# Optimization experiments

Hardware: AMD Instinct MI355X
Metric: run time of the kernel (lower is better)

## Reference

```python
import jax, jax.numpy as jnp
import numpy as np

N = 100000   # num_nodes
E = 1600000  # num_edges (avg degree 16)
IN = 128     # input_dim
H = 4        # num_heads
D = 32       # hidden_dim per head (H*D == 128)
NEG_SLOPE = 0.2


def setup_inputs() -> dict:
    key = jax.random.key(0)
    ks = jax.random.split(key, 8)
    s = 0.1
    x = jax.random.normal(ks[0], (N, IN), jnp.float32)
    edge_index = jax.random.randint(ks[1], (2, E), 0, N, dtype=jnp.int32)
    W_gat = jax.random.normal(ks[2], (H * D, IN), jnp.float32) * s   # GATConv lin weight
    att_src = jax.random.normal(ks[3], (H, D), jnp.float32) * s
    att_dst = jax.random.normal(ks[4], (H, D), jnp.float32) * s
    bias_gat = jnp.zeros((H * D,), jnp.float32)
    W_lin = jax.random.normal(ks[5], (IN, H * D), jnp.float32) * s   # nn.Linear weight
    b_lin = jnp.zeros((IN,), jnp.float32)
    return {"x": x, "edge_index": edge_index, "W_gat": W_gat,
            "att_src": att_src, "att_dst": att_dst, "bias_gat": bias_gat,
            "W_lin": W_lin, "b_lin": b_lin}


def reference(x, edge_index, W_gat, att_src, att_dst, bias_gat, W_lin, b_lin):
    # (eval mode: all dropouts are identity; sparse edge weights unused in original)
    h = (x @ W_gat.T).reshape(N, H, D)                 # [N,H,D] per-head projections
    a_s = jnp.einsum('nhd,hd->nh', h, att_src)         # [N,H]
    a_d = jnp.einsum('nhd,hd->nh', h, att_dst)         # [N,H]
    # add self loops (PyG default)
    loop = jnp.arange(N, dtype=edge_index.dtype)
    src = jnp.concatenate([edge_index[0], loop])       # [E+N]
    dst = jnp.concatenate([edge_index[1], loop])       # [E+N]
    logits = jax.nn.leaky_relu(a_s[src] + a_d[dst], NEG_SLOPE)  # [E+N,H]
    # segment softmax over edges grouped by destination node
    m = jax.ops.segment_max(logits, dst, num_segments=N)        # [N,H]
    e = jnp.exp(logits - m[dst])
    denom = jax.ops.segment_sum(e, dst, num_segments=N)         # [N,H]
    alpha = e / denom[dst]                                      # [E+N,H]
    # scatter-aggregate weighted source features
    agg = jax.ops.segment_sum(alpha[:, :, None] * h[src], dst, num_segments=N)
    out = agg.reshape(N, H * D) + bias_gat             # concat heads + bias
    out = jax.nn.relu(out)
    return out @ W_lin.T + b_lin                       # [N, IN]
```

## Files before the change

### kernel.cpp

```cpp
#include <hip/hip_runtime.h>
#include <hip/hip_bf16.h>
#include <hip/hip_fp16.h>

#define NN 100000
#define EE 1600000
#define INF_DIM 128
#define NHEAD 4
#define HDIM 32
#define NEG_SLOPE 0.2f

#define GB 1024

typedef __attribute__((ext_vector_type(8))) short short8;
typedef __attribute__((ext_vector_type(4))) float floatx4;

__device__ __forceinline__ unsigned int cvtpk_bf16(float lo, float hi) {
  unsigned int r;
  asm("v_cvt_pk_bf16_f32 %0, %1, %2" : "=v"(r) : "v"(lo), "v"(hi));
  return r;
}
__device__ __forceinline__ unsigned int packh2(float a, float b) {
  const __half ha = __float2half(a), hb = __float2half(b);
  const unsigned short ua = *(const unsigned short*)&ha;
  const unsigned short ub = *(const unsigned short*)&hb;
  return (unsigned int)ua | ((unsigned int)ub << 16);
}
__device__ __forceinline__ float pickw(const int4 e, const int head) {
  const unsigned int d = (head & 2) ? (unsigned int)e.z : (unsigned int)e.y;
  const unsigned short us =
      (head & 1) ? (unsigned short)(d >> 16) : (unsigned short)(d & 0xffffu);
  const __half h = *(const __half*)&us;
  return __half2float(h);
}
__device__ __forceinline__ void accum8h(const uint4 g, const float c,
                                        float* acc) {
  union { uint4 u; __half2 h[4]; } v;
  v.u = g;
#pragma unroll
  for (int j = 0; j < 4; ++j) {
    const float2 f = __half22float2(v.h[j]);
    acc[2 * j] = fmaf(c, f.x, acc[2 * j]);
    acc[2 * j + 1] = fmaf(c, f.y, acc[2 * j + 1]);
  }
}

#define LDA 136

__global__ __launch_bounds__(256) void gemm_mfma(
    const float* __restrict__ Af, const unsigned short* __restrict__ Ab,
    const float* __restrict__ W, const float* __restrict__ bias,
    unsigned short* __restrict__ Ch, float* __restrict__ Cf,
    const float* __restrict__ att_src, const float* __restrict__ att_dst,
    float* __restrict__ a_s, float* __restrict__ a_d,
    const int* __restrict__ dstE, int* __restrict__ deg8, int M) {
  __shared__ unsigned short sW[128 * LDA];
  const int tid = threadIdx.x;

  if (dstE) {
    int* mydeg = deg8 + (size_t)(blockIdx.x & 7) * NN;
    for (int e = blockIdx.x * 256 + tid; e < EE; e += GB * 256)
      atomicAdd(&mydeg[dstE[e]], 1);
  }

  {
    const int r = tid >> 1;
    const int c0 = (tid & 1) * 64;
#pragma unroll
    for (int j = 0; j < 16; ++j) {
      const float4 v = *(const float4*)&W[r * 128 + c0 + j * 4];
      uint2 u;
      u.x = cvtpk_bf16(v.x, v.y);
      u.y = cvtpk_bf16(v.z, v.w);
      *(uint2*)&sW[r * LDA + c0 + j * 4] = u;
    }
  }
  __syncthreads();

  const int wv = tid >> 6;
  const int lane = tid & 63;
  const int l16 = lane & 15;
  const int quad = lane >> 4;
  const int ntiles = (M + 63) >> 6;

  float avs[8], avd[8];
  if (a_s) {
#pragma unroll
    for (int nt = 0; nt < 8; ++nt) {
      avs[nt] = att_src[nt * 16 + l16];
      avd[nt] = att_dst[nt * 16 + l16];
    }
  }

  const unsigned short* wBase = &sW[l16 * LDA + quad * 8];

  for (int t = blockIdx.x; t < ntiles; t += GB) {
    const int m0 = t * 64;
    const int arow = m0 + wv * 16 + l16;
    const int arowc = arow < M ? arow : M - 1;

    short8 af[4];
    if (Af) {
      const float* ap = &Af[(size_t)arowc * 128 + quad * 8];
#pragma unroll
      for (int kc = 0; kc < 4; ++kc) {
        const float4 v0 = *(const float4*)(ap + kc * 32);
        const float4 v1 = *(const float4*)(ap + kc * 32 + 4);
        union { uint4 u; short8 s; } c;
        c.u.x = cvtpk_bf16(v0.x, v0.y);
        c.u.y = cvtpk_bf16(v0.z, v0.w);
        c.u.z = cvtpk_bf16(v1.x, v1.y);
        c.u.w = cvtpk_bf16(v1.z, v1.w);
        af[kc] = c.s;
      }
    } else {
      const unsigned short* ap = &Ab[(size_t)arowc * 128 + quad * 8];
#pragma unroll
      for (int kc = 0; kc < 4; ++kc) af[kc] = *(const short8*)(ap + kc * 32);
    }

    floatx4 acc[8];
#pragma unroll
    for (int i = 0; i < 8; ++i) acc[i] = (floatx4){0.f, 0.f, 0.f, 0.f};

#pragma unroll
    for (int kc = 0; kc < 4; ++kc) {
#pragma unroll
      for (int nt = 0; nt < 8; ++nt) {
        const short8 bfrag = *(const short8*)(wBase + nt * 16 * LDA + kc * 32);
        acc[nt] = __builtin_amdgcn_mfma_f32_16x16x32_bf16(af[kc], bfrag,
                                                          acc[nt], 0, 0, 0);
      }
    }

    const int mrow = m0 + wv * 16 + quad * 4;
#pragma unroll
    for (int nt = 0; nt < 8; ++nt) {
      const int col = nt * 16 + l16;
      const float bv = Cf ? bias[col] : 0.f;
#pragma unroll
      for (int r = 0; r < 4; ++r) {
        const int gm = mrow + r;
        if (gm < M) {
          const float v = acc[nt][r];
          if (Ch) {
            const __half hh = __float2half(v);
            Ch[(size_t)gm * 128 + col] = *(const unsigned short*)&hh;
          } else {
            Cf[(size_t)gm * 128 + col] = v + bv;
          }
        }
      }
    }

    if (a_s) {
#pragma unroll
      for (int r = 0; r < 4; ++r) {
        float ps0 = acc[0][r] * avs[0] + acc[1][r] * avs[1];
        float ps1 = acc[2][r] * avs[2] + acc[3][r] * avs[3];
        float ps2 = acc[4][r] * avs[4] + acc[5][r] * avs[5];
        float ps3 = acc[6][r] * avs[6] + acc[7][r] * avs[7];
        float pd0 = acc[0][r] * avd[0] + acc[1][r] * avd[1];
        float pd1 = acc[2][r] * avd[2] + acc[3][r] * avd[3];
        float pd2 = acc[4][r] * avd[4] + acc[5][r] * avd[5];
        float pd3 = acc[6][r] * avd[6] + acc[7][r] * avd[7];
#pragma unroll
        for (int off = 1; off < 16; off <<= 1) {
          ps0 += __shfl_xor(ps0, off);
          ps1 += __shfl_xor(ps1, off);
          ps2 += __shfl_xor(ps2, off);
          ps3 += __shfl_xor(ps3, off);
          pd0 += __shfl_xor(pd0, off);
          pd1 += __shfl_xor(pd1, off);
          pd2 += __shfl_xor(pd2, off);
          pd3 += __shfl_xor(pd3, off);
        }
        const int gm = mrow + r;
        if (gm < M) {
          const int hs = l16 & 3;
          float vs = ps0;
          if (hs == 1) vs = ps1;
          if (hs == 2) vs = ps2;
          if (hs == 3) vs = ps3;
          float vd = pd0;
          if (hs == 1) vd = pd1;
          if (hs == 2) vd = pd2;
          if (hs == 3) vd = pd3;
          if (l16 < 4)
            a_s[gm * 4 + hs] = vs;
          else if (l16 < 8)
            a_d[gm * 4 + hs] = vd;
        }
      }
    }
  }
}

__global__ __launch_bounds__(256) void alloc_kernel(
    const int* __restrict__ deg8, int* __restrict__ deg,
    int* __restrict__ rowptr, int* __restrict__ cur,
    int* __restrict__ counter) {
  const int i = blockIdx.x * blockDim.x + threadIdx.x;
  const int lane = threadIdx.x & 63;
  int d = 0;
  if (i < NN) {
#pragma unroll
    for (int k = 0; k < 8; ++k) d += deg8[(size_t)k * NN + i];
  }
  int s = d;
#pragma unroll
  for (int off = 1; off < 64; off <<= 1) {
    const int v = __shfl_up(s, off, 64);
    if (lane >= off) s += v;
  }
  const int total = __shfl(s, 63, 64);
  int base = 0;
  if (lane == 63) base = atomicAdd(counter, total);
  base = __shfl(base, 63, 64);
  const int p = base + s - d;
  if (i < NN) {
    rowptr[i] = p;
    cur[i] = p;
    deg[i] = d;
  }
}

__global__ void scatter_kernel(const int* __restrict__ src,
                               const int* __restrict__ dst,
                               const float* __restrict__ a_s,
                               const float* __restrict__ a_d,
                               int* __restrict__ cur, int4* __restrict__ ebuf) {
  const int iA = blockIdx.x * blockDim.x + threadIdx.x;
  const int iB = iA + (EE / 2);
  const int sA_ = src[iA];
  const int dA = dst[iA];
  const int sB_ = src[iB];
  const int dB = dst[iB];
  const int pA = atomicAdd(&cur[dA], 1);
  const int pB = atomicAdd(&cur[dB], 1);
  const float4 asA = *(const float4*)&a_s[sA_ * 4];
  const float4 adA = *(const float4*)&a_d[dA * 4];
  const float4 asB = *(const float4*)&a_s[sB_ * 4];
  const float4 adB = *(const float4*)&a_d[dB * 4];
  float4 lA, lB;
  lA.x = asA.x + adA.x;
  lA.y = asA.y + adA.y;
  lA.z = asA.z + adA.z;
  lA.w = asA.w + adA.w;
  lB.x = asB.x + adB.x;
  lB.y = asB.y + adB.y;
  lB.z = asB.z + adB.z;
  lB.w = asB.w + adB.w;
  lA.x = lA.x > 0.f ? lA.x : NEG_SLOPE * lA.x;
  lA.y = lA.y > 0.f ? lA.y : NEG_SLOPE * lA.y;
  lA.z = lA.z > 0.f ? lA.z : NEG_SLOPE * lA.z;
  lA.w = lA.w > 0.f ? lA.w : NEG_SLOPE * lA.w;
  lB.x = lB.x > 0.f ? lB.x : NEG_SLOPE * lB.x;
  lB.y = lB.y > 0.f ? lB.y : NEG_SLOPE * lB.y;
  lB.z = lB.z > 0.f ? lB.z : NEG_SLOPE * lB.z;
  lB.w = lB.w > 0.f ? lB.w : NEG_SLOPE * lB.w;
  int4 eA, eB;
  eA.x = sA_;
  eA.y = (int)packh2(__expf(lA.x), __expf(lA.y));
  eA.z = (int)packh2(__expf(lA.z), __expf(lA.w));
  eA.w = 0;
  eB.x = sB_;
  eB.y = (int)packh2(__expf(lB.x), __expf(lB.y));
  eB.z = (int)packh2(__expf(lB.z), __expf(lB.w));
  eB.w = 0;
  ebuf[pA] = eA;
  ebuf[pB] = eB;
}

__global__ __launch_bounds__(256) void aggregate_kernel(
    const uint4* __restrict__ hbd4, const float* __restrict__ a_s,
    const float* __restrict__ a_d, const float* __restrict__ bias_gat,
    const int* __restrict__ rowptr, const int* __restrict__ deg,
    const int4* __restrict__ ebuf, uint4* __restrict__ obd4) {
  const int wave = (blockIdx.x * blockDim.x + threadIdx.x) >> 6;
  if (wave >= NN) return;
  const int lane = threadIdx.x & 63;
  const int q = lane >> 4;
  const int f = lane & 15;
  const int head = f >> 2;
  const int n = wave;

  float acc[8];
  float ds;
  {
    const float l0 = a_s[n * 4 + head] + a_d[n * 4 + head];
    const float l = fmaxf(l0, NEG_SLOPE * l0);
    float cs = __expf(l);
    if (q != 0) cs = 0.f;
    union { uint4 u; __half2 h[4]; } v;
    v.u = hbd4[(size_t)n * 16 + f];
#pragma unroll
    for (int j = 0; j < 4; ++j) {
      const float2 fv = __half22float2(v.h[j]);
      acc[2 * j] = cs * fv.x;
      acc[2 * j + 1] = cs * fv.y;
    }
    ds = cs;
  }

  const int beg = rowptr[n];
  const int end = beg + deg[n];
  for (int i = beg; i < end; i += 16) {
    int4 e0, e1, e2, e3;
    {
      const int i0 = i + q, i1 = i + 4 + q, i2 = i + 8 + q, i3 = i + 12 + q;
      e0 = ebuf[i0 < end ? i0 : end - 1];
      e1 = ebuf[i1 < end ? i1 : end - 1];
      e2 = ebuf[i2 < end ? i2 : end - 1];
      e3 = ebuf[i3 < end ? i3 : end - 1];
    }
    const uint4 g0 = hbd4[(size_t)e0.x * 16 + f];
    const uint4 g1 = hbd4[(size_t)e1.x * 16 + f];
    const uint4 g2 = hbd4[(size_t)e2.x * 16 + f];
    const uint4 g3 = hbd4[(size_t)e3.x * 16 + f];
    float c0 = pickw(e0, head);
    float c1 = pickw(e1, head);
    float c2 = pickw(e2, head);
    float c3 = pickw(e3, head);
    if (i + q >= end) c0 = 0.f;
    if (i + 4 + q >= end) c1 = 0.f;
    if (i + 8 + q >= end) c2 = 0.f;
    if (i + 12 + q >= end) c3 = 0.f;
    accum8h(g0, c0, acc);
    accum8h(g1, c1, acc);
    accum8h(g2, c2, acc);
    accum8h(g3, c3, acc);
    ds += c0 + c1 + c2 + c3;
  }

#pragma unroll
  for (int j = 0; j < 8; ++j) {
    acc[j] += __shfl_xor(acc[j], 16);
    acc[j] += __shfl_xor(acc[j], 32);
  }
  ds += __shfl_xor(ds, 16);
  ds += __shfl_xor(ds, 32);

  if (q == 0) {
    const float inv = 1.0f / ds;
    const float4 b0 = *(const float4*)&bias_gat[f * 8];
    const float4 b1 = *(const float4*)&bias_gat[f * 8 + 4];
    float v0 = acc[0] * inv + b0.x;
    float v1 = acc[1] * inv + b0.y;
    float v2 = acc[2] * inv + b0.z;
    float v3 = acc[3] * inv + b0.w;
    float v4 = acc[4] * inv + b1.x;
    float v5 = acc[5] * inv + b1.y;
    float v6 = acc[6] * inv + b1.z;
    float v7 = acc[7] * inv + b1.w;
    v0 = v0 > 0.f ? v0 : 0.f;
    v1 = v1 > 0.f ? v1 : 0.f;
    v2 = v2 > 0.f ? v2 : 0.f;
    v3 = v3 > 0.f ? v3 : 0.f;
    v4 = v4 > 0.f ? v4 : 0.f;
    v5 = v5 > 0.f ? v5 : 0.f;
    v6 = v6 > 0.f ? v6 : 0.f;
    v7 = v7 > 0.f ? v7 : 0.f;
    uint4 r;
    r.x = cvtpk_bf16(v0, v1);
    r.y = cvtpk_bf16(v2, v3);
    r.z = cvtpk_bf16(v4, v5);
    r.w = cvtpk_bf16(v6, v7);
    obd4[(size_t)n * 16 + f] = r;
  }
}

extern "C" void kernel_launch(void* const* d_in, const int* in_sizes, int n_in,
                              void* d_out, int out_size, void* d_ws,
                              size_t ws_size, hipStream_t stream) {
  const float* x = (const float*)d_in[0];
  const int* ei = (const int*)d_in[1];
  const float* W_gat = (const float*)d_in[2];
  const float* att_src = (const float*)d_in[3];
  const float* att_dst = (const float*)d_in[4];
  const float* bias_gat = (const float*)d_in[5];
  const float* W_lin = (const float*)d_in[6];
  const float* b_lin = (const float*)d_in[7];
  float* out = (float*)d_out;

  char* ws = (char*)d_ws;
  size_t off = 0;
  unsigned short* hb = (unsigned short*)(ws + off);
  off += (size_t)NN * 128 * 2;
  unsigned short* ob = (unsigned short*)(ws + off);
  off += (size_t)NN * 128 * 2;
  float* a_s = (float*)(ws + off); off += (size_t)NN * 4 * 4;
  float* a_d = (float*)(ws + off); off += (size_t)NN * 4 * 4;
  int* deg8 = (int*)(ws + off); off += (size_t)8 * NN * 4;
  int* deg = (int*)(ws + off); off += (size_t)NN * 4;
  int* rowptr = (int*)(ws + off); off += (size_t)(NN + 4) * 4;
  int* cur = (int*)(ws + off); off += (size_t)NN * 4;
  int* counter = (int*)(ws + off); off += 16;
  int4* ebuf = (int4*)(ws + off); off += (size_t)EE * 16;

  const int* src = ei;
  const int* dst = ei + EE;

  hipMemsetAsync(deg8, 0, (size_t)8 * NN * 4, stream);
  hipMemsetAsync(counter, 0, 16, stream);
  gemm_mfma<<<GB, 256, 0, stream>>>(x, nullptr, W_gat, nullptr, hb, nullptr,
                                    att_src, att_dst, a_s, a_d, dst, deg8, NN);
  alloc_kernel<<<(NN + 255) / 256, 256, 0, stream>>>(deg8, deg, rowptr, cur,
                                                     counter);
  scatter_kernel<<<(EE / 2 + 255) / 256, 256, 0, stream>>>(src, dst, a_s, a_d,
                                                           cur, ebuf);
  aggregate_kernel<<<(NN + 3) / 4, 256, 0, stream>>>(
      (const uint4*)hb, a_s, a_d, bias_gat, rowptr, deg, ebuf,
      (uint4*)ob);
  gemm_mfma<<<GB, 256, 0, stream>>>(nullptr, ob, W_lin, b_lin, nullptr, out,
                                    nullptr, nullptr, nullptr, nullptr,
                                    nullptr, nullptr, NN);
}
```

Before: 381.4 us.

## Build CSR with per-slice LDS histograms and deterministic scatter offsets

Replaces the global-atomic degree counting and cursor-based scatter with a two-pass counting sort. Each block histograms one slice of the edges for half the node range into LDS, using packed 8-bit counters. A prefix kernel turns these into per-slice offsets plus rowptr/deg. The scatter then uses LDS atomics instead of global atomics on cur. The edge order becomes deterministic and contention on global atomics goes away, at the cost of an extra launch, a 25 MB count buffer, and each block reading its slice of dst twice (once per node half).

```diff
diff --git a/kernel.cpp b/kernel.cpp
--- a/kernel.cpp
+++ b/kernel.cpp
@@ -10,6 +10,11 @@
 #define NEG_SLOPE 0.2f
 
 #define GB 1024
+#define SLICES 256
+#define EPS 6250
+#define HALFN 50000
+#define HQ4 12500
+#define NN4 25000
 
 typedef __attribute__((ext_vector_type(8))) short short8;
 typedef __attribute__((ext_vector_type(4))) float floatx4;
@@ -51,16 +56,9 @@
     const float* __restrict__ W, const float* __restrict__ bias,
     unsigned short* __restrict__ Ch, float* __restrict__ Cf,
     const float* __restrict__ att_src, const float* __restrict__ att_dst,
-    float* __restrict__ a_s, float* __restrict__ a_d,
-    const int* __restrict__ dstE, int* __restrict__ deg8, int M) {
+    float* __restrict__ a_s, float* __restrict__ a_d, int M) {
   __shared__ unsigned short sW[128 * LDA];
   const int tid = threadIdx.x;
-
-  if (dstE) {
-    int* mydeg = deg8 + (size_t)(blockIdx.x & 7) * NN;
-    for (int e = blockIdx.x * 256 + tid; e < EE; e += GB * 256)
-      atomicAdd(&mydeg[dstE[e]], 1);
-  }
 
   {
     const int r = tid >> 1;
@@ -195,80 +193,112 @@
   }
 }
 
+__global__ __launch_bounds__(256) void hist_kernel(const int* __restrict__ dst,
+                                                   unsigned int* __restrict__ cnt4) {
+  __shared__ unsigned int h[HQ4];
+  const int s = blockIdx.x >> 1;
+  const int half = blockIdx.x & 1;
+  const int tid = threadIdx.x;
+  for (int j = tid; j < HQ4; j += 256) h[j] = 0u;
+  __syncthreads();
+  const int lo = half * HALFN;
+  for (int i = s * EPS + tid; i < (s + 1) * EPS; i += 256) {
+    const int d = dst[i] - lo;
+    if ((unsigned)d < (unsigned)HALFN)
+      atomicAdd(&h[d >> 2], 1u << ((d & 3) * 8));
+  }
+  __syncthreads();
+  unsigned int* out = cnt4 + (size_t)s * NN4 + half * HQ4;
+  for (int j = tid; j < HQ4; j += 256) out[j] = h[j];
+}
+
 __global__ __launch_bounds__(256) void alloc_kernel(
-    const int* __restrict__ deg8, int* __restrict__ deg,
-    int* __restrict__ rowptr, int* __restrict__ cur,
-    int* __restrict__ counter) {
-  const int i = blockIdx.x * blockDim.x + threadIdx.x;
+    unsigned int* __restrict__ cnt4, int* __restrict__ deg,
+    int* __restrict__ rowptr, int* __restrict__ counter) {
+  const int n4 = blockIdx.x * blockDim.x + threadIdx.x;
   const int lane = threadIdx.x & 63;
-  int d = 0;
-  if (i < NN) {
-#pragma unroll
-    for (int k = 0; k < 8; ++k) d += deg8[(size_t)k * NN + i];
-  }
-  int s = d;
+  unsigned int run = 0;
+  if (n4 < NN4) {
+    for (int sb = 0; sb < SLICES; sb += 16) {
+      unsigned int c[16];
+#pragma unroll
+      for (int k = 0; k < 16; ++k)
+        c[k] = cnt4[(size_t)(sb + k) * NN4 + n4];
+#pragma unroll
+      for (int k = 0; k < 16; ++k) {
+        cnt4[(size_t)(sb + k) * NN4 + n4] = run;
+        run += c[k];
+      }
+    }
+  }
+  const int d0 = run & 0xff;
+  const int d1 = (run >> 8) & 0xff;
+  const int d2 = (run >> 16) & 0xff;
+  const int d3 = (int)(run >> 24);
+  const int t = d0 + d1 + d2 + d3;
+  int sc = t;
 #pragma unroll
   for (int off = 1; off < 64; off <<= 1) {
-    const int v = __shfl_up(s, off, 64);
-    if (lane >= off) s += v;
-  }
-  const int total = __shfl(s, 63, 64);
+    const int v = __shfl_up(sc, off, 64);
+    if (lane >= off) sc += v;
+  }
+  const int total = __shfl(sc, 63, 64);
   int base = 0;
   if (lane == 63) base = atomicAdd(counter, total);
   base = __shfl(base, 63, 64);
-  const int p = base + s - d;
-  if (i < NN) {
-    rowptr[i] = p;
-    cur[i] = p;
-    deg[i] = d;
-  }
-}
-
-__global__ void scatter_kernel(const int* __restrict__ src,
-                               const int* __restrict__ dst,
-                               const float* __restrict__ a_s,
-                               const float* __restrict__ a_d,
-                               int* __restrict__ cur, int4* __restrict__ ebuf) {
-  const int iA = blockIdx.x * blockDim.x + threadIdx.x;
-  const int iB = iA + (EE / 2);
-  const int sA_ = src[iA];
-  const int dA = dst[iA];
-  const int sB_ = src[iB];
-  const int dB = dst[iB];
-  const int pA = atomicAdd(&cur[dA], 1);
-  const int pB = atomicAdd(&cur[dB], 1);
-  const float4 asA = *(const float4*)&a_s[sA_ * 4];
-  const float4 adA = *(const float4*)&a_d[dA * 4];
-  const float4 asB = *(const float4*)&a_s[sB_ * 4];
-  const float4 adB = *(const float4*)&a_d[dB * 4];
-  float4 lA, lB;
-  lA.x = asA.x + adA.x;
-  lA.y = asA.y + adA.y;
-  lA.z = asA.z + adA.z;
-  lA.w = asA.w + adA.w;
-  lB.x = asB.x + adB.x;
-  lB.y = asB.y + adB.y;
-  lB.z = asB.z + adB.z;
-  lB.w = asB.w + adB.w;
-  lA.x = lA.x > 0.f ? lA.x : NEG_SLOPE * lA.x;
-  lA.y = lA.y > 0.f ? lA.y : NEG_SLOPE * lA.y;
-  lA.z = lA.z > 0.f ? lA.z : NEG_SLOPE * lA.z;
-  lA.w = lA.w > 0.f ? lA.w : NEG_SLOPE * lA.w;
-  lB.x = lB.x > 0.f ? lB.x : NEG_SLOPE * lB.x;
-  lB.y = lB.y > 0.f ? lB.y : NEG_SLOPE * lB.y;
-  lB.z = lB.z > 0.f ? lB.z : NEG_SLOPE * lB.z;
-  lB.w = lB.w > 0.f ? lB.w : NEG_SLOPE * lB.w;
-  int4 eA, eB;
-  eA.x = sA_;
-  eA.y = (int)packh2(__expf(lA.x), __expf(lA.y));
-  eA.z = (int)packh2(__expf(lA.z), __expf(lA.w));
-  eA.w = 0;
-  eB.x = sB_;
-  eB.y = (int)packh2(__expf(lB.x), __expf(lB.y));
-  eB.z = (int)packh2(__expf(lB.z), __expf(lB.w));
-  eB.w = 0;
-  ebuf[pA] = eA;
-  ebuf[pB] = eB;
+  const int p = base + sc - t;
+  if (n4 < NN4) {
+    const int n = n4 * 4;
+    rowptr[n] = p;
+    rowptr[n + 1] = p + d0;
+    rowptr[n + 2] = p + d0 + d1;
+    rowptr[n + 3] = p + d0 + d1 + d2;
+    deg[n] = d0;
+    deg[n + 1] = d1;
+    deg[n + 2] = d2;
+    deg[n + 3] = d3;
+  }
+}
+
+__global__ __launch_bounds__(256) void scatter_kernel(
+    const int* __restrict__ src, const int* __restrict__ dst,
+    const float* __restrict__ a_s, const float* __restrict__ a_d,
+    const unsigned int* __restrict__ cnt4, const int* __restrict__ rowptr,
+    int4* __restrict__ ebuf) {
+  __shared__ unsigned int h[HQ4];
+  const int s = blockIdx.x >> 1;
+  const int half = blockIdx.x & 1;
+  const int tid = threadIdx.x;
+  const unsigned int* basep = cnt4 + (size_t)s * NN4 + half * HQ4;
+  for (int j = tid; j < HQ4; j += 256) h[j] = basep[j];
+  __syncthreads();
+  const int lo = half * HALFN;
+  for (int i = s * EPS + tid; i < (s + 1) * EPS; i += 256) {
+    const int d = dst[i];
+    const int dl = d - lo;
+    if ((unsigned)dl >= (unsigned)HALFN) continue;
+    const int sr = src[i];
+    const unsigned int sh = (dl & 3) * 8;
+    const unsigned int old = atomicAdd(&h[dl >> 2], 1u << sh);
+    const int p = rowptr[d] + (int)((old >> sh) & 0xffu);
+    const float4 as = *(const float4*)&a_s[sr * 4];
+    const float4 ad = *(const float4*)&a_d[d * 4];
+    float4 l;
+    l.x = as.x + ad.x;
+    l.y = as.y + ad.y;
+    l.z = as.z + ad.z;
+    l.w = as.w + ad.w;
+    l.x = l.x > 0.f ? l.x : NEG_SLOPE * l.x;
+    l.y = l.y > 0.f ? l.y : NEG_SLOPE * l.y;
+    l.z = l.z > 0.f ? l.z : NEG_SLOPE * l.z;
+    l.w = l.w > 0.f ? l.w : NEG_SLOPE * l.w;
+    int4 e;
+    e.x = sr;
+    e.y = (int)packh2(__expf(l.x), __expf(l.y));
+    e.z = (int)packh2(__expf(l.z), __expf(l.w));
+    e.w = 0;
+    ebuf[p] = e;
+  }
 }
 
 __global__ __launch_bounds__(256) void aggregate_kernel(
@@ -390,28 +420,27 @@
   off += (size_t)NN * 128 * 2;
   float* a_s = (float*)(ws + off); off += (size_t)NN * 4 * 4;
   float* a_d = (float*)(ws + off); off += (size_t)NN * 4 * 4;
-  int* deg8 = (int*)(ws + off); off += (size_t)8 * NN * 4;
+  unsigned int* cnt4 = (unsigned int*)(ws + off);
+  off += (size_t)SLICES * NN4 * 4;
   int* deg = (int*)(ws + off); off += (size_t)NN * 4;
   int* rowptr = (int*)(ws + off); off += (size_t)(NN + 4) * 4;
-  int* cur = (int*)(ws + off); off += (size_t)NN * 4;
   int* counter = (int*)(ws + off); off += 16;
   int4* ebuf = (int4*)(ws + off); off += (size_t)EE * 16;
 
   const int* src = ei;
   const int* dst = ei + EE;
 
-  hipMemsetAsync(deg8, 0, (size_t)8 * NN * 4, stream);
   hipMemsetAsync(counter, 0, 16, stream);
+  hist_kernel<<<SLICES * 2, 256, 0, stream>>>(dst, cnt4);
+  alloc_kernel<<<(NN4 + 255) / 256, 256, 0, stream>>>(cnt4, deg, rowptr,
+                                                      counter);
   gemm_mfma<<<GB, 256, 0, stream>>>(x, nullptr, W_gat, nullptr, hb, nullptr,
-                                    att_src, att_dst, a_s, a_d, dst, deg8, NN);
-  alloc_kernel<<<(NN + 255) / 256, 256, 0, stream>>>(deg8, deg, rowptr, cur,
-                                                     counter);
-  scatter_kernel<<<(EE / 2 + 255) / 256, 256, 0, stream>>>(src, dst, a_s, a_d,
-                                                           cur, ebuf);
+                                    att_src, att_dst, a_s, a_d, NN);
+  scatter_kernel<<<SLICES * 2, 256, 0, stream>>>(src, dst, a_s, a_d, cnt4,
+                                                 rowptr, ebuf);
   aggregate_kernel<<<(NN + 3) / 4, 256, 0, stream>>>(
       (const uint4*)hb, a_s, a_d, bias_gat, rowptr, deg, ebuf,
       (uint4*)ob);
   gemm_mfma<<<GB, 256, 0, stream>>>(nullptr, ob, W_lin, b_lin, nullptr, out,
-                                    nullptr, nullptr, nullptr, nullptr,
-                                    nullptr, nullptr, NN);
-}
+                                    nullptr, nullptr, nullptr, nullptr, NN);
+}
```

Result: faster. 325.5 us (-14.7%).
